# Performance work log

Hardware: AMD Instinct MI355X
Metric: run time of the kernel (lower is better)

Reference implementation:

```python
import jax, jax.numpy as jnp
import numpy as np

N_REP = 8      # N: repeated gelu(LN(linear)) blocks
M_LAYERS = 4   # M: transformer encoder layers
SEQ = 100
D = 4
FF = 2048      # PyTorch TransformerEncoderLayer default dim_feedforward
H = 4          # nhead; head_dim = 1


def _ln(x, g, b, axes):
    m = jnp.mean(x, axis=axes, keepdims=True)
    v = jnp.var(x, axis=axes, keepdims=True)
    return (x - m) / jnp.sqrt(v + 1e-5) * g + b


def _encoder_layer(x, Win, bi, Wout, bout, W1, b1, W2, b2, g1, be1, g2, be2):
    # x: [S, Nb, D] with S = batch_size (batch_first=False!), Nb = 100
    S, Nb, E = x.shape
    qkv = x @ Win.T + bi                      # [S, Nb, 3D]
    q, k, v = jnp.split(qkv, 3, axis=-1)
    qh = q.reshape(S, Nb, H, E // H)          # head_dim = 1, scale 1/sqrt(1)=1
    kh = k.reshape(S, Nb, H, E // H)
    vh = v.reshape(S, Nb, H, E // H)
    scores = jnp.einsum('snhd,tnhd->nhst', qh, kh)   # [Nb, H, S, S]
    attn = jax.nn.softmax(scores, axis=-1)
    o = jnp.einsum('nhst,tnhd->snhd', attn, vh).reshape(S, Nb, E)
    o = o @ Wout.T + bout
    x = _ln(x + o, g1, be1, (-1,))            # post-norm (norm_first=False)
    f = jax.nn.relu(x @ W1.T + b1) @ W2.T + b2
    return _ln(x + f, g2, be2, (-1,))


def setup_inputs() -> dict:
    key = jax.random.key(0)
    ks = jax.random.split(key, 24)
    B = 256
    d = {}
    d['x'] = jax.random.normal(ks[0], (B, SEQ, D), dtype=jnp.float32)
    # conv1: kernel_size=1, 1->1 channel -> scalar affine
    d['conv_w'] = jax.random.normal(ks[1], (), dtype=jnp.float32) * 0.5 + 1.0
    d['conv_b'] = jax.random.normal(ks[2], (), dtype=jnp.float32) * 0.1
    # shared 4x4 linear (self.liner) and LayerNorm([100,4])
    d['Wl'] = jax.random.normal(ks[3], (D, D), dtype=jnp.float32) * 0.5
    d['bl'] = jax.random.normal(ks[4], (D,), dtype=jnp.float32) * 0.1
    d['ln_g'] = jnp.ones((SEQ, D), dtype=jnp.float32)
    d['ln_b'] = jnp.zeros((SEQ, D), dtype=jnp.float32)
    # transformer encoder params, stacked over M layers
    s = 0.3
    d['Win'] = jax.random.normal(ks[5], (M_LAYERS, 3 * D, D), dtype=jnp.float32) * s
    d['bi'] = jax.random.normal(ks[6], (M_LAYERS, 3 * D), dtype=jnp.float32) * 0.05
    d['Wout'] = jax.random.normal(ks[7], (M_LAYERS, D, D), dtype=jnp.float32) * s
    d['bout'] = jax.random.normal(ks[8], (M_LAYERS, D), dtype=jnp.float32) * 0.05
    d['W1'] = jax.random.normal(ks[9], (M_LAYERS, FF, D), dtype=jnp.float32) * 0.05
    d['b1'] = jax.random.normal(ks[10], (M_LAYERS, FF), dtype=jnp.float32) * 0.05
    d['W2'] = jax.random.normal(ks[11], (M_LAYERS, D, FF), dtype=jnp.float32) * 0.02
    d['b2'] = jax.random.normal(ks[12], (M_LAYERS, D), dtype=jnp.float32) * 0.05
    d['g1'] = jnp.ones((M_LAYERS, D), dtype=jnp.float32)
    d['be1'] = jnp.zeros((M_LAYERS, D), dtype=jnp.float32)
    d['g2'] = jnp.ones((M_LAYERS, D), dtype=jnp.float32)
    d['be2'] = jnp.zeros((M_LAYERS, D), dtype=jnp.float32)
    return d


def reference(x, conv_w, conv_b, Wl, bl, ln_g, ln_b,
              Win, bi, Wout, bout, W1, b1, W2, b2, g1, be1, g2, be2):
    # per-channel kernel_size=1 conv == elementwise affine (same scalar for all 4 channels)
    h = x * conv_w + conv_b                   # [B, 100, 4]
    for _ in range(N_REP):
        h = jax.nn.gelu(_ln(h @ Wl.T + bl, ln_g, ln_b, (-2, -1)), approximate=False)
    h = h @ Wl.T + bl
    for i in range(M_LAYERS):
        h = _encoder_layer(h, Win[i], bi[i], Wout[i], bout[i], W1[i], b1[i],
                           W2[i], b2[i], g1[i], be1[i], g2[i], be2[i])
    h = h @ Wl.T + bl
    return jax.nn.softmax(h, axis=2)
```

## Files before the change

### kernel.cpp

```cpp
#include <hip/hip_runtime.h>
#include <math.h>

#define SEQ 100
#define BATCH 256
#define NREP 8
#define FFDIM 2048

__device__ __forceinline__ float wave_sum64(float v) {
    #pragma unroll
    for (int o = 32; o > 0; o >>= 1) v += __shfl_xor(v, o, 64);
    return v;
}

__global__ __launch_bounds__(128) void k_stageA(
    const float* __restrict__ x, const float* __restrict__ convw,
    const float* __restrict__ convb, const float* __restrict__ Wl,
    const float* __restrict__ bl, const float* __restrict__ lng,
    const float* __restrict__ lnb, float* __restrict__ X)
{
    const int b = blockIdx.x;
    const int r = threadIdx.x;
    const bool act = (r < SEQ);
    __shared__ float red[2][2];

    const float cw = convw[0], cb = convb[0];
    float W[4][4], B[4];
    #pragma unroll
    for (int j = 0; j < 4; ++j) {
        B[j] = bl[j];
        #pragma unroll
        for (int d = 0; d < 4; ++d) W[j][d] = Wl[j * 4 + d];
    }

    float h[4] = {0.f, 0.f, 0.f, 0.f};
    float g4[4] = {0.f, 0.f, 0.f, 0.f}, b4[4] = {0.f, 0.f, 0.f, 0.f};
    if (act) {
        float4 xr = *(const float4*)(x + (b * SEQ + r) * 4);
        h[0] = fmaf(xr.x, cw, cb); h[1] = fmaf(xr.y, cw, cb);
        h[2] = fmaf(xr.z, cw, cb); h[3] = fmaf(xr.w, cw, cb);
        float4 g = *(const float4*)(lng + r * 4);
        float4 bb = *(const float4*)(lnb + r * 4);
        g4[0] = g.x; g4[1] = g.y; g4[2] = g.z; g4[3] = g.w;
        b4[0] = bb.x; b4[1] = bb.y; b4[2] = bb.z; b4[3] = bb.w;
    }

    for (int it = 0; it < NREP; ++it) {
        float y[4] = {0.f, 0.f, 0.f, 0.f};
        float s1 = 0.f, s2 = 0.f;
        if (act) {
            #pragma unroll
            for (int j = 0; j < 4; ++j) {
                float yy = B[j];
                #pragma unroll
                for (int d = 0; d < 4; ++d) yy = fmaf(h[d], W[j][d], yy);
                y[j] = yy; s1 += yy; s2 = fmaf(yy, yy, s2);
            }
        }
        s1 = wave_sum64(s1);
        s2 = wave_sum64(s2);
        const int wid = threadIdx.x >> 6;
        if ((threadIdx.x & 63) == 0) { red[wid][0] = s1; red[wid][1] = s2; }
        __syncthreads();
        const float tS = red[0][0] + red[1][0];
        const float tQ = red[0][1] + red[1][1];
        __syncthreads();
        const float mean = tS * (1.0f / 400.0f);
        const float var  = tQ * (1.0f / 400.0f) - mean * mean;
        const float rstd = rsqrtf(var + 1e-5f);
        if (act) {
            #pragma unroll
            for (int j = 0; j < 4; ++j) {
                float v = fmaf((y[j] - mean) * rstd, g4[j], b4[j]);
                h[j] = 0.5f * v * (1.0f + erff(v * 0.70710678118654752f));
            }
        }
    }
    if (act) {
        float y[4];
        #pragma unroll
        for (int j = 0; j < 4; ++j) {
            float yy = B[j];
            #pragma unroll
            for (int d = 0; d < 4; ++d) yy = fmaf(h[d], W[j][d], yy);
            y[j] = yy;
        }
        *(float4*)(X + (b * SEQ + r) * 4) = make_float4(y[0], y[1], y[2], y[3]);
    }
}

__global__ __launch_bounds__(256) void k_attn(
    const float* __restrict__ X, float* __restrict__ O,
    const float* __restrict__ Win, const float* __restrict__ bi)
{
    const int n  = blockIdx.x;
    const int hd = blockIdx.y;
    const int s  = threadIdx.x;
    __shared__ float2 kv[256];
    __shared__ float red[4][2];

    float4 xr = *(const float4*)(X + (s * SEQ + n) * 4);
    const float* wq = Win + hd * 4;
    const float* wk = Win + (4 + hd) * 4;
    const float* wv = Win + (8 + hd) * 4;
    float q = bi[hd]     + xr.x*wq[0] + xr.y*wq[1] + xr.z*wq[2] + xr.w*wq[3];
    float k = bi[4 + hd] + xr.x*wk[0] + xr.y*wk[1] + xr.z*wk[2] + xr.w*wk[3];
    float v = bi[8 + hd] + xr.x*wv[0] + xr.y*wv[1] + xr.z*wv[2] + xr.w*wv[3];
    kv[s] = make_float2(k, v);

    float kmx = k, kmn = k;
    #pragma unroll
    for (int o = 32; o > 0; o >>= 1) {
        kmx = fmaxf(kmx, __shfl_xor(kmx, o, 64));
        kmn = fminf(kmn, __shfl_xor(kmn, o, 64));
    }
    const int wid = s >> 6;
    if ((s & 63) == 0) { red[wid][0] = kmx; red[wid][1] = kmn; }
    __syncthreads();
    kmx = fmaxf(fmaxf(red[0][0], red[1][0]), fmaxf(red[2][0], red[3][0]));
    kmn = fminf(fminf(red[0][1], red[1][1]), fminf(red[2][1], red[3][1]));

    const float m = (q >= 0.f) ? q * kmx : q * kmn;
    float den = 0.f, num = 0.f;
    #pragma unroll 8
    for (int t = 0; t < 256; ++t) {
        float2 kvt = kv[t];
        float p = __expf(fmaf(q, kvt.x, -m));
        den += p;
        num = fmaf(p, kvt.y, num);
    }
    O[(s * SEQ + n) * 4 + hd] = num / den;
}

__global__ __launch_bounds__(1024) void k_ffn(
    float* __restrict__ X, const float* __restrict__ O,
    const float* __restrict__ Wout, const float* __restrict__ bout,
    const float* __restrict__ W1, const float* __restrict__ b1,
    const float* __restrict__ W2, const float* __restrict__ b2,
    const float* __restrict__ g1, const float* __restrict__ be1,
    const float* __restrict__ g2, const float* __restrict__ be2)
{
    __shared__ float x1s[64][4];
    __shared__ float pacc[16][64][4];
    const int wid  = threadIdx.x >> 6;
    const int lane = threadIdx.x & 63;

    if (wid == 0) {
        const int g = blockIdx.x * 64 + lane;
        float4 xr = *(const float4*)(X + g * 4);
        float4 orow = *(const float4*)(O + g * 4);
        float xv[4] = {xr.x, xr.y, xr.z, xr.w};
        float ov[4] = {orow.x, orow.y, orow.z, orow.w};
        float rr[4];
        #pragma unroll
        for (int d = 0; d < 4; ++d) {
            float op = bout[d];
            #pragma unroll
            for (int e = 0; e < 4; ++e) op = fmaf(ov[e], Wout[d * 4 + e], op);
            rr[d] = xv[d] + op;
        }
        float mean = 0.25f * (rr[0] + rr[1] + rr[2] + rr[3]);
        float var = 0.f;
        #pragma unroll
        for (int d = 0; d < 4; ++d) { float dv = rr[d] - mean; var = fmaf(dv, dv, var); }
        float rstd = rsqrtf(0.25f * var + 1e-5f);
        #pragma unroll
        for (int d = 0; d < 4; ++d)
            x1s[lane][d] = fmaf((rr[d] - mean) * rstd, g1[d], be1[d]);
    }
    __syncthreads();

    const float x0 = x1s[lane][0], x1_ = x1s[lane][1];
    const float x2_ = x1s[lane][2], x3_ = x1s[lane][3];
    float a0 = 0.f, a1 = 0.f, a2 = 0.f, a3 = 0.f;
    const int fbase = __builtin_amdgcn_readfirstlane(wid) * 128;
    #pragma unroll 4
    for (int j = 0; j < 128; ++j) {
        const int f = fbase + j;
        const float w0 = W1[f * 4 + 0], w1 = W1[f * 4 + 1];
        const float w2 = W1[f * 4 + 2], w3 = W1[f * 4 + 3];
        float hh = b1[f];
        hh = fmaf(x0, w0, hh); hh = fmaf(x1_, w1, hh);
        hh = fmaf(x2_, w2, hh); hh = fmaf(x3_, w3, hh);
        hh = fmaxf(hh, 0.f);
        a0 = fmaf(hh, W2[0 * FFDIM + f], a0);
        a1 = fmaf(hh, W2[1 * FFDIM + f], a1);
        a2 = fmaf(hh, W2[2 * FFDIM + f], a2);
        a3 = fmaf(hh, W2[3 * FFDIM + f], a3);
    }
    pacc[wid][lane][0] = a0; pacc[wid][lane][1] = a1;
    pacc[wid][lane][2] = a2; pacc[wid][lane][3] = a3;
    __syncthreads();

    if (threadIdx.x < 256) {
        const int r = threadIdx.x >> 2, d = threadIdx.x & 3;
        float s = b2[d];
        #pragma unroll
        for (int w = 0; w < 16; ++w) s += pacc[w][r][d];
        float val = x1s[r][d] + s;
        float sum = val + __shfl_xor(val, 1, 64);
        sum += __shfl_xor(sum, 2, 64);
        const float mean = 0.25f * sum;
        const float dv = val - mean;
        float qq = dv * dv;
        float qs = qq + __shfl_xor(qq, 1, 64);
        qs += __shfl_xor(qs, 2, 64);
        const float rstd = rsqrtf(0.25f * qs + 1e-5f);
        X[(blockIdx.x * 64 + r) * 4 + d] = fmaf(dv * rstd, g2[d], be2[d]);
    }
}

__global__ __launch_bounds__(256) void k_final(
    const float* __restrict__ X, const float* __restrict__ Wl,
    const float* __restrict__ bl, float* __restrict__ out)
{
    const int g = blockIdx.x * 256 + threadIdx.x;
    float4 xr = *(const float4*)(X + g * 4);
    float xv[4] = {xr.x, xr.y, xr.z, xr.w};
    float y[4];
    #pragma unroll
    for (int j = 0; j < 4; ++j) {
        float yy = bl[j];
        #pragma unroll
        for (int d = 0; d < 4; ++d) yy = fmaf(xv[d], Wl[j * 4 + d], yy);
        y[j] = yy;
    }
    float m = fmaxf(fmaxf(y[0], y[1]), fmaxf(y[2], y[3]));
    float e[4], s = 0.f;
    #pragma unroll
    for (int j = 0; j < 4; ++j) { e[j] = __expf(y[j] - m); s += e[j]; }
    const float inv = 1.0f / s;
    *(float4*)(out + g * 4) =
        make_float4(e[0] * inv, e[1] * inv, e[2] * inv, e[3] * inv);
}

extern "C" void kernel_launch(void* const* d_in, const int* in_sizes, int n_in,
                              void* d_out, int out_size, void* d_ws, size_t ws_size,
                              hipStream_t stream)
{
    const float* x     = (const float*)d_in[0];
    const float* convw = (const float*)d_in[1];
    const float* convb = (const float*)d_in[2];
    const float* Wl    = (const float*)d_in[3];
    const float* bl    = (const float*)d_in[4];
    const float* lng   = (const float*)d_in[5];
    const float* lnb   = (const float*)d_in[6];
    const float* Win   = (const float*)d_in[7];
    const float* bi    = (const float*)d_in[8];
    const float* Wout  = (const float*)d_in[9];
    const float* bout  = (const float*)d_in[10];
    const float* W1    = (const float*)d_in[11];
    const float* b1    = (const float*)d_in[12];
    const float* W2    = (const float*)d_in[13];
    const float* b2    = (const float*)d_in[14];
    const float* g1    = (const float*)d_in[15];
    const float* be1   = (const float*)d_in[16];
    const float* g2    = (const float*)d_in[17];
    const float* be2   = (const float*)d_in[18];

    float* X = (float*)d_ws;
    float* O = X + BATCH * SEQ * 4;
    float* out = (float*)d_out;

    k_stageA<<<BATCH, 128, 0, stream>>>(x, convw, convb, Wl, bl, lng, lnb, X);
    for (int l = 0; l < 4; ++l) {
        k_attn<<<dim3(SEQ, 4), 256, 0, stream>>>(X, O, Win + l * 48, bi + l * 12);
        k_ffn<<<400, 1024, 0, stream>>>(X, O,
            Wout + l * 16, bout + l * 4,
            W1 + l * FFDIM * 4, b1 + l * FFDIM,
            W2 + l * 4 * FFDIM, b2 + l * 4,
            g1 + l * 4, be1 + l * 4, g2 + l * 4, be2 + l * 4);
    }
    k_final<<<SEQ, 256, 0, stream>>>(X, Wl, bl, out);
}
```

Before: 128.0 us.

## Fuse all stages into one persistent kernel with software grid barriers

Replaces the ten separate kernel launches (stage A, four attention plus FFN pairs, final softmax) with a single persistent kernel of 256 blocks that separates phases with an atomic-counter grid barrier. Stage A now uses a single wave with two rows per lane, so no block-level reduction is needed. Attention slots and FFN rows are remapped so each block handles up to two attention slots and 100 rows, with two rows per lane in the FFN. This removes launch gaps and the per-launch tail, at the cost of spin-wait barriers, the assumption that all 256 blocks are co-resident, and fewer blocks in the FFN phase (256 instead of 400).

```diff
diff --git a/kernel.cpp b/kernel.cpp
--- a/kernel.cpp
+++ b/kernel.cpp
@@ -1,274 +1,312 @@
 #include <hip/hip_runtime.h>
 #include <math.h>
 
-#define SEQ 100
-#define BATCH 256
-#define NREP 8
-#define FFDIM 2048
-
-__device__ __forceinline__ float wave_sum64(float v) {
-    #pragma unroll
-    for (int o = 32; o > 0; o >>= 1) v += __shfl_xor(v, o, 64);
-    return v;
+#define SEQ   100
+#define NREP  8
+#define FFD   2048
+#define NBLK  256
+#define RSQRT2 0.70710678118654752440f
+
+__device__ __forceinline__ float wsum(float v) {
+#pragma unroll
+  for (int o = 32; o > 0; o >>= 1) v += __shfl_xor(v, o, 64);
+  return v;
 }
 
-__global__ __launch_bounds__(128) void k_stageA(
-    const float* __restrict__ x, const float* __restrict__ convw,
-    const float* __restrict__ convb, const float* __restrict__ Wl,
-    const float* __restrict__ bl, const float* __restrict__ lng,
-    const float* __restrict__ lnb, float* __restrict__ X)
+__device__ __forceinline__ void gbar(unsigned* cnt, unsigned* gen) {
+  __syncthreads();
+  if (threadIdx.x == 0) {
+    __threadfence();
+    unsigned g0 = __hip_atomic_load(gen, __ATOMIC_RELAXED, __HIP_MEMORY_SCOPE_AGENT);
+    unsigned a  = __hip_atomic_fetch_add(cnt, 1u, __ATOMIC_ACQ_REL, __HIP_MEMORY_SCOPE_AGENT);
+    if (a == (unsigned)(NBLK - 1)) {
+      __hip_atomic_store(cnt, 0u, __ATOMIC_RELAXED, __HIP_MEMORY_SCOPE_AGENT);
+      __hip_atomic_fetch_add(gen, 1u, __ATOMIC_RELEASE, __HIP_MEMORY_SCOPE_AGENT);
+    } else {
+      while (__hip_atomic_load(gen, __ATOMIC_ACQUIRE, __HIP_MEMORY_SCOPE_AGENT) == g0)
+        __builtin_amdgcn_s_sleep(2);
+    }
+    __threadfence();
+  }
+  __syncthreads();
+}
+
+__global__ __launch_bounds__(1024) void k_fused(
+    const float* __restrict__ x,
+    const float* __restrict__ convw, const float* __restrict__ convb,
+    const float* __restrict__ Wl,  const float* __restrict__ bl,
+    const float* __restrict__ lng, const float* __restrict__ lnb,
+    const float* __restrict__ Win, const float* __restrict__ bi,
+    const float* __restrict__ Wout,const float* __restrict__ bout,
+    const float* __restrict__ W1,  const float* __restrict__ b1,
+    const float* __restrict__ W2,  const float* __restrict__ b2,
+    const float* __restrict__ g1,  const float* __restrict__ be1,
+    const float* __restrict__ g2,  const float* __restrict__ be2,
+    float* __restrict__ X, float* __restrict__ O,
+    unsigned* __restrict__ barc, unsigned* __restrict__ barg,
+    float* __restrict__ out)
 {
-    const int b = blockIdx.x;
-    const int r = threadIdx.x;
-    const bool act = (r < SEQ);
-    __shared__ float red[2][2];
-
+  __shared__ float2 kvs[4][256];
+  __shared__ float  kred[4][4][2];
+  __shared__ float  x1s[100][4];
+  __shared__ float  pacc[16][100][4];
+
+  const int t    = threadIdx.x;
+  const int b    = blockIdx.x;
+  const int lane = t & 63;
+  const int wv   = t >> 6;
+
+  if (t < 64) {
     const float cw = convw[0], cb = convb[0];
     float W[4][4], B[4];
-    #pragma unroll
+#pragma unroll
     for (int j = 0; j < 4; ++j) {
-        B[j] = bl[j];
-        #pragma unroll
-        for (int d = 0; d < 4; ++d) W[j][d] = Wl[j * 4 + d];
-    }
-
-    float h[4] = {0.f, 0.f, 0.f, 0.f};
-    float g4[4] = {0.f, 0.f, 0.f, 0.f}, b4[4] = {0.f, 0.f, 0.f, 0.f};
+      B[j] = bl[j];
+#pragma unroll
+      for (int d = 0; d < 4; ++d) W[j][d] = Wl[j * 4 + d];
+    }
+    const bool act = lane < 50;
+    float h[2][4] = {{0.f,0.f,0.f,0.f},{0.f,0.f,0.f,0.f}};
+    float gg[2][4] = {{0.f}}, eb[2][4] = {{0.f}};
     if (act) {
+#pragma unroll
+      for (int p = 0; p < 2; ++p) {
+        const int r = lane * 2 + p;
         float4 xr = *(const float4*)(x + (b * SEQ + r) * 4);
-        h[0] = fmaf(xr.x, cw, cb); h[1] = fmaf(xr.y, cw, cb);
-        h[2] = fmaf(xr.z, cw, cb); h[3] = fmaf(xr.w, cw, cb);
-        float4 g = *(const float4*)(lng + r * 4);
-        float4 bb = *(const float4*)(lnb + r * 4);
-        g4[0] = g.x; g4[1] = g.y; g4[2] = g.z; g4[3] = g.w;
-        b4[0] = bb.x; b4[1] = bb.y; b4[2] = bb.z; b4[3] = bb.w;
-    }
-
+        h[p][0] = fmaf(xr.x, cw, cb); h[p][1] = fmaf(xr.y, cw, cb);
+        h[p][2] = fmaf(xr.z, cw, cb); h[p][3] = fmaf(xr.w, cw, cb);
+        float4 gv = *(const float4*)(lng + r * 4);
+        float4 bv = *(const float4*)(lnb + r * 4);
+        gg[p][0] = gv.x; gg[p][1] = gv.y; gg[p][2] = gv.z; gg[p][3] = gv.w;
+        eb[p][0] = bv.x; eb[p][1] = bv.y; eb[p][2] = bv.z; eb[p][3] = bv.w;
+      }
+    }
     for (int it = 0; it < NREP; ++it) {
-        float y[4] = {0.f, 0.f, 0.f, 0.f};
-        float s1 = 0.f, s2 = 0.f;
-        if (act) {
-            #pragma unroll
-            for (int j = 0; j < 4; ++j) {
-                float yy = B[j];
-                #pragma unroll
-                for (int d = 0; d < 4; ++d) yy = fmaf(h[d], W[j][d], yy);
-                y[j] = yy; s1 += yy; s2 = fmaf(yy, yy, s2);
-            }
+      float y[2][4] = {{0.f,0.f,0.f,0.f},{0.f,0.f,0.f,0.f}};
+      float s1 = 0.f, s2 = 0.f;
+      if (act) {
+#pragma unroll
+        for (int p = 0; p < 2; ++p)
+#pragma unroll
+          for (int j = 0; j < 4; ++j) {
+            float yy = B[j];
+#pragma unroll
+            for (int d = 0; d < 4; ++d) yy = fmaf(h[p][d], W[j][d], yy);
+            y[p][j] = yy; s1 += yy; s2 = fmaf(yy, yy, s2);
+          }
+      }
+      s1 = wsum(s1); s2 = wsum(s2);
+      const float mean = s1 * (1.0f / 400.0f);
+      const float var  = s2 * (1.0f / 400.0f) - mean * mean;
+      const float rstd = rsqrtf(var + 1e-5f);
+      if (act) {
+#pragma unroll
+        for (int p = 0; p < 2; ++p)
+#pragma unroll
+          for (int j = 0; j < 4; ++j) {
+            float vv = fmaf((y[p][j] - mean) * rstd, gg[p][j], eb[p][j]);
+            h[p][j] = 0.5f * vv * (1.0f + erff(vv * RSQRT2));
+          }
+      }
+    }
+    if (act) {
+#pragma unroll
+      for (int p = 0; p < 2; ++p) {
+        float yy[4];
+#pragma unroll
+        for (int j = 0; j < 4; ++j) {
+          float a = B[j];
+#pragma unroll
+          for (int d = 0; d < 4; ++d) a = fmaf(h[p][d], W[j][d], a);
+          yy[j] = a;
         }
-        s1 = wave_sum64(s1);
-        s2 = wave_sum64(s2);
-        const int wid = threadIdx.x >> 6;
-        if ((threadIdx.x & 63) == 0) { red[wid][0] = s1; red[wid][1] = s2; }
-        __syncthreads();
-        const float tS = red[0][0] + red[1][0];
-        const float tQ = red[0][1] + red[1][1];
-        __syncthreads();
-        const float mean = tS * (1.0f / 400.0f);
-        const float var  = tQ * (1.0f / 400.0f) - mean * mean;
-        const float rstd = rsqrtf(var + 1e-5f);
-        if (act) {
-            #pragma unroll
-            for (int j = 0; j < 4; ++j) {
-                float v = fmaf((y[j] - mean) * rstd, g4[j], b4[j]);
-                h[j] = 0.5f * v * (1.0f + erff(v * 0.70710678118654752f));
-            }
-        }
-    }
-    if (act) {
-        float y[4];
-        #pragma unroll
-        for (int j = 0; j < 4; ++j) {
-            float yy = B[j];
-            #pragma unroll
-            for (int d = 0; d < 4; ++d) yy = fmaf(h[d], W[j][d], yy);
-            y[j] = yy;
-        }
-        *(float4*)(X + (b * SEQ + r) * 4) = make_float4(y[0], y[1], y[2], y[3]);
-    }
-}
-
-__global__ __launch_bounds__(256) void k_attn(
-    const float* __restrict__ X, float* __restrict__ O,
-    const float* __restrict__ Win, const float* __restrict__ bi)
-{
-    const int n  = blockIdx.x;
-    const int hd = blockIdx.y;
-    const int s  = threadIdx.x;
-    __shared__ float2 kv[256];
-    __shared__ float red[4][2];
-
-    float4 xr = *(const float4*)(X + (s * SEQ + n) * 4);
-    const float* wq = Win + hd * 4;
-    const float* wk = Win + (4 + hd) * 4;
-    const float* wv = Win + (8 + hd) * 4;
-    float q = bi[hd]     + xr.x*wq[0] + xr.y*wq[1] + xr.z*wq[2] + xr.w*wq[3];
-    float k = bi[4 + hd] + xr.x*wk[0] + xr.y*wk[1] + xr.z*wk[2] + xr.w*wk[3];
-    float v = bi[8 + hd] + xr.x*wv[0] + xr.y*wv[1] + xr.z*wv[2] + xr.w*wv[3];
-    kv[s] = make_float2(k, v);
-
-    float kmx = k, kmn = k;
-    #pragma unroll
-    for (int o = 32; o > 0; o >>= 1) {
+        *(float4*)(X + (b * SEQ + lane * 2 + p) * 4) =
+            make_float4(yy[0], yy[1], yy[2], yy[3]);
+      }
+    }
+  }
+  gbar(barc, barg);
+
+  for (int l = 0; l < 4; ++l) {
+    {
+      const float* Wa = Win + l * 48;
+      const float* ba = bi + l * 12;
+      const int g    = t >> 8;
+      const int s    = t & 255;
+      const int slot = b + 256 * g;
+      const int sc   = slot < 400 ? slot : 399;
+      const int n    = sc % 100;
+      const int hd   = sc / 100;
+      float4 xr = *(const float4*)(X + (s * SEQ + n) * 4);
+      const float* wq = Wa + hd * 4;
+      const float* wk = Wa + (4 + hd) * 4;
+      const float* wvp = Wa + (8 + hd) * 4;
+      float q = ba[hd]   + xr.x*wq[0] + xr.y*wq[1] + xr.z*wq[2] + xr.w*wq[3];
+      float k = ba[4+hd] + xr.x*wk[0] + xr.y*wk[1] + xr.z*wk[2] + xr.w*wk[3];
+      float v = ba[8+hd] + xr.x*wvp[0]+ xr.y*wvp[1]+ xr.z*wvp[2]+ xr.w*wvp[3];
+      kvs[g][s] = make_float2(k, v);
+      float kmx = k, kmn = k;
+#pragma unroll
+      for (int o = 32; o > 0; o >>= 1) {
         kmx = fmaxf(kmx, __shfl_xor(kmx, o, 64));
         kmn = fminf(kmn, __shfl_xor(kmn, o, 64));
-    }
-    const int wid = s >> 6;
-    if ((s & 63) == 0) { red[wid][0] = kmx; red[wid][1] = kmn; }
-    __syncthreads();
-    kmx = fmaxf(fmaxf(red[0][0], red[1][0]), fmaxf(red[2][0], red[3][0]));
-    kmn = fminf(fminf(red[0][1], red[1][1]), fminf(red[2][1], red[3][1]));
-
-    const float m = (q >= 0.f) ? q * kmx : q * kmn;
-    float den = 0.f, num = 0.f;
-    #pragma unroll 8
-    for (int t = 0; t < 256; ++t) {
-        float2 kvt = kv[t];
-        float p = __expf(fmaf(q, kvt.x, -m));
-        den += p;
-        num = fmaf(p, kvt.y, num);
-    }
-    O[(s * SEQ + n) * 4 + hd] = num / den;
-}
-
-__global__ __launch_bounds__(1024) void k_ffn(
-    float* __restrict__ X, const float* __restrict__ O,
-    const float* __restrict__ Wout, const float* __restrict__ bout,
-    const float* __restrict__ W1, const float* __restrict__ b1,
-    const float* __restrict__ W2, const float* __restrict__ b2,
-    const float* __restrict__ g1, const float* __restrict__ be1,
-    const float* __restrict__ g2, const float* __restrict__ be2)
-{
-    __shared__ float x1s[64][4];
-    __shared__ float pacc[16][64][4];
-    const int wid  = threadIdx.x >> 6;
-    const int lane = threadIdx.x & 63;
-
-    if (wid == 0) {
-        const int g = blockIdx.x * 64 + lane;
-        float4 xr = *(const float4*)(X + g * 4);
-        float4 orow = *(const float4*)(O + g * 4);
+      }
+      if ((t & 63) == 0) { kred[g][(t >> 6) & 3][0] = kmx; kred[g][(t >> 6) & 3][1] = kmn; }
+      __syncthreads();
+      if (slot < 400) {
+        kmx = fmaxf(fmaxf(kred[g][0][0], kred[g][1][0]),
+                    fmaxf(kred[g][2][0], kred[g][3][0]));
+        kmn = fminf(fminf(kred[g][0][1], kred[g][1][1]),
+                    fminf(kred[g][2][1], kred[g][3][1]));
+        const float m = (q >= 0.f) ? q * kmx : q * kmn;
+        float den = 0.f, num = 0.f;
+#pragma unroll 8
+        for (int t2 = 0; t2 < 256; ++t2) {
+          float2 kt = kvs[g][t2];
+          float p = __expf(fmaf(q, kt.x, -m));
+          den += p;
+          num = fmaf(p, kt.y, num);
+        }
+        O[(s * SEQ + n) * 4 + hd] = num / den;
+      }
+    }
+    gbar(barc, barg);
+
+    {
+      const float* W1l = W1 + l * FFD * 4;
+      const float* b1l = b1 + l * FFD;
+      const float* W2l = W2 + l * 4 * FFD;
+      const float* b2l = b2 + l * 4;
+      const float* Wo  = Wout + l * 16;
+      const float* bo  = bout + l * 4;
+      const float* g1l = g1 + l * 4;  const float* e1l = be1 + l * 4;
+      const float* g2l = g2 + l * 4;  const float* e2l = be2 + l * 4;
+
+      if (t < 100) {
+        const int gr = b * SEQ + t;
+        float4 xr = *(const float4*)(X + gr * 4);
+        float4 od = *(const float4*)(O + gr * 4);
         float xv[4] = {xr.x, xr.y, xr.z, xr.w};
-        float ov[4] = {orow.x, orow.y, orow.z, orow.w};
+        float ov[4] = {od.x, od.y, od.z, od.w};
         float rr[4];
-        #pragma unroll
+#pragma unroll
         for (int d = 0; d < 4; ++d) {
-            float op = bout[d];
-            #pragma unroll
-            for (int e = 0; e < 4; ++e) op = fmaf(ov[e], Wout[d * 4 + e], op);
-            rr[d] = xv[d] + op;
+          float op = bo[d];
+#pragma unroll
+          for (int e = 0; e < 4; ++e) op = fmaf(ov[e], Wo[d * 4 + e], op);
+          rr[d] = xv[d] + op;
         }
         float mean = 0.25f * (rr[0] + rr[1] + rr[2] + rr[3]);
         float var = 0.f;
-        #pragma unroll
+#pragma unroll
         for (int d = 0; d < 4; ++d) { float dv = rr[d] - mean; var = fmaf(dv, dv, var); }
         float rstd = rsqrtf(0.25f * var + 1e-5f);
-        #pragma unroll
+#pragma unroll
         for (int d = 0; d < 4; ++d)
-            x1s[lane][d] = fmaf((rr[d] - mean) * rstd, g1[d], be1[d]);
-    }
-    __syncthreads();
-
-    const float x0 = x1s[lane][0], x1_ = x1s[lane][1];
-    const float x2_ = x1s[lane][2], x3_ = x1s[lane][3];
-    float a0 = 0.f, a1 = 0.f, a2 = 0.f, a3 = 0.f;
-    const int fbase = __builtin_amdgcn_readfirstlane(wid) * 128;
-    #pragma unroll 4
-    for (int j = 0; j < 128; ++j) {
-        const int f = fbase + j;
-        const float w0 = W1[f * 4 + 0], w1 = W1[f * 4 + 1];
-        const float w2 = W1[f * 4 + 2], w3 = W1[f * 4 + 3];
-        float hh = b1[f];
-        hh = fmaf(x0, w0, hh); hh = fmaf(x1_, w1, hh);
-        hh = fmaf(x2_, w2, hh); hh = fmaf(x3_, w3, hh);
-        hh = fmaxf(hh, 0.f);
-        a0 = fmaf(hh, W2[0 * FFDIM + f], a0);
-        a1 = fmaf(hh, W2[1 * FFDIM + f], a1);
-        a2 = fmaf(hh, W2[2 * FFDIM + f], a2);
-        a3 = fmaf(hh, W2[3 * FFDIM + f], a3);
-    }
-    pacc[wid][lane][0] = a0; pacc[wid][lane][1] = a1;
-    pacc[wid][lane][2] = a2; pacc[wid][lane][3] = a3;
-    __syncthreads();
-
-    if (threadIdx.x < 256) {
-        const int r = threadIdx.x >> 2, d = threadIdx.x & 3;
-        float s = b2[d];
-        #pragma unroll
-        for (int w = 0; w < 16; ++w) s += pacc[w][r][d];
-        float val = x1s[r][d] + s;
-        float sum = val + __shfl_xor(val, 1, 64);
-        sum += __shfl_xor(sum, 2, 64);
+          x1s[t][d] = fmaf((rr[d] - mean) * rstd, g1l[d], e1l[d]);
+      }
+      __syncthreads();
+
+      const int fb = __builtin_amdgcn_readfirstlane(wv) * 128;
+      const int rB = 64 + (lane < 36 ? lane : 35);
+      const float xA0 = x1s[lane][0], xA1 = x1s[lane][1];
+      const float xA2 = x1s[lane][2], xA3 = x1s[lane][3];
+      const float xB0 = x1s[rB][0], xB1 = x1s[rB][1];
+      const float xB2 = x1s[rB][2], xB3 = x1s[rB][3];
+      float aA0=0.f,aA1=0.f,aA2=0.f,aA3=0.f;
+      float aB0=0.f,aB1=0.f,aB2=0.f,aB3=0.f;
+#pragma unroll 4
+      for (int j = 0; j < 128; ++j) {
+        const int f = fb + j;
+        const float4 w1v = *(const float4*)(W1l + f * 4);
+        const float bb  = b1l[f];
+        const float w20 = W2l[f],           w21 = W2l[FFD + f];
+        const float w22 = W2l[2 * FFD + f], w23 = W2l[3 * FFD + f];
+        float hA = fmaf(xA3, w1v.w, fmaf(xA2, w1v.z, fmaf(xA1, w1v.y, fmaf(xA0, w1v.x, bb))));
+        hA = fmaxf(hA, 0.f);
+        aA0 = fmaf(hA, w20, aA0); aA1 = fmaf(hA, w21, aA1);
+        aA2 = fmaf(hA, w22, aA2); aA3 = fmaf(hA, w23, aA3);
+        float hB = fmaf(xB3, w1v.w, fmaf(xB2, w1v.z, fmaf(xB1, w1v.y, fmaf(xB0, w1v.x, bb))));
+        hB = fmaxf(hB, 0.f);
+        aB0 = fmaf(hB, w20, aB0); aB1 = fmaf(hB, w21, aB1);
+        aB2 = fmaf(hB, w22, aB2); aB3 = fmaf(hB, w23, aB3);
+      }
+      *(float4*)&pacc[wv][lane][0] = make_float4(aA0, aA1, aA2, aA3);
+      if (lane < 36)
+        *(float4*)&pacc[wv][64 + lane][0] = make_float4(aB0, aB1, aB2, aB3);
+      __syncthreads();
+
+      if (t < 400) {
+        const int r = t >> 2, d = t & 3;
+        float sacc = b2l[d];
+#pragma unroll
+        for (int w = 0; w < 16; ++w) sacc += pacc[w][r][d];
+        float val = x1s[r][d] + sacc;
+        float sum = val + __shfl_xor(val, 1, 64); sum += __shfl_xor(sum, 2, 64);
         const float mean = 0.25f * sum;
         const float dv = val - mean;
         float qq = dv * dv;
-        float qs = qq + __shfl_xor(qq, 1, 64);
-        qs += __shfl_xor(qs, 2, 64);
+        float qs = qq + __shfl_xor(qq, 1, 64); qs += __shfl_xor(qs, 2, 64);
         const float rstd = rsqrtf(0.25f * qs + 1e-5f);
-        X[(blockIdx.x * 64 + r) * 4 + d] = fmaf(dv * rstd, g2[d], be2[d]);
-    }
-}
-
-__global__ __launch_bounds__(256) void k_final(
-    const float* __restrict__ X, const float* __restrict__ Wl,
-    const float* __restrict__ bl, float* __restrict__ out)
-{
-    const int g = blockIdx.x * 256 + threadIdx.x;
-    float4 xr = *(const float4*)(X + g * 4);
+        X[(b * SEQ + r) * 4 + d] = fmaf(dv * rstd, g2l[d], e2l[d]);
+      }
+    }
+    if (l < 3) gbar(barc, barg);
+    else __syncthreads();
+  }
+
+  if (t < 100) {
+    const int gr = b * SEQ + t;
+    float4 xr = *(const float4*)(X + gr * 4);
     float xv[4] = {xr.x, xr.y, xr.z, xr.w};
     float y[4];
-    #pragma unroll
+#pragma unroll
     for (int j = 0; j < 4; ++j) {
-        float yy = bl[j];
-        #pragma unroll
-        for (int d = 0; d < 4; ++d) yy = fmaf(xv[d], Wl[j * 4 + d], yy);
-        y[j] = yy;
+      float yy = bl[j];
+#pragma unroll
+      for (int d = 0; d < 4; ++d) yy = fmaf(xv[d], Wl[j * 4 + d], yy);
+      y[j] = yy;
     }
     float m = fmaxf(fmaxf(y[0], y[1]), fmaxf(y[2], y[3]));
     float e[4], s = 0.f;
-    #pragma unroll
+#pragma unroll
     for (int j = 0; j < 4; ++j) { e[j] = __expf(y[j] - m); s += e[j]; }
     const float inv = 1.0f / s;
-    *(float4*)(out + g * 4) =
-        make_float4(e[0] * inv, e[1] * inv, e[2] * inv, e[3] * inv);
+    *(float4*)(out + gr * 4) = make_float4(e[0]*inv, e[1]*inv, e[2]*inv, e[3]*inv);
+  }
 }
 
 extern "C" void kernel_launch(void* const* d_in, const int* in_sizes, int n_in,
                               void* d_out, int out_size, void* d_ws, size_t ws_size,
                               hipStream_t stream)
 {
-    const float* x     = (const float*)d_in[0];
-    const float* convw = (const float*)d_in[1];
-    const float* convb = (const float*)d_in[2];
-    const float* Wl    = (const float*)d_in[3];
-    const float* bl    = (const float*)d_in[4];
-    const float* lng   = (const float*)d_in[5];
-    const float* lnb   = (const float*)d_in[6];
-    const float* Win   = (const float*)d_in[7];
-    const float* bi    = (const float*)d_in[8];
-    const float* Wout  = (const float*)d_in[9];
-    const float* bout  = (const float*)d_in[10];
-    const float* W1    = (const float*)d_in[11];
-    const float* b1    = (const float*)d_in[12];
-    const float* W2    = (const float*)d_in[13];
-    const float* b2    = (const float*)d_in[14];
-    const float* g1    = (const float*)d_in[15];
-    const float* be1   = (const float*)d_in[16];
-    const float* g2    = (const float*)d_in[17];
-    const float* be2   = (const float*)d_in[18];
-
-    float* X = (float*)d_ws;
-    float* O = X + BATCH * SEQ * 4;
-    float* out = (float*)d_out;
-
-    k_stageA<<<BATCH, 128, 0, stream>>>(x, convw, convb, Wl, bl, lng, lnb, X);
-    for (int l = 0; l < 4; ++l) {
-        k_attn<<<dim3(SEQ, 4), 256, 0, stream>>>(X, O, Win + l * 48, bi + l * 12);
-        k_ffn<<<400, 1024, 0, stream>>>(X, O,
-            Wout + l * 16, bout + l * 4,
-            W1 + l * FFDIM * 4, b1 + l * FFDIM,
-            W2 + l * 4 * FFDIM, b2 + l * 4,
-            g1 + l * 4, be1 + l * 4, g2 + l * 4, be2 + l * 4);
-    }
-    k_final<<<SEQ, 256, 0, stream>>>(X, Wl, bl, out);
+  const float* x     = (const float*)d_in[0];
+  const float* convw = (const float*)d_in[1];
+  const float* convb = (const float*)d_in[2];
+  const float* Wl    = (const float*)d_in[3];
+  const float* bl    = (const float*)d_in[4];
+  const float* lng   = (const float*)d_in[5];
+  const float* lnb   = (const float*)d_in[6];
+  const float* Win   = (const float*)d_in[7];
+  const float* bi    = (const float*)d_in[8];
+  const float* Wout  = (const float*)d_in[9];
+  const float* bout  = (const float*)d_in[10];
+  const float* W1    = (const float*)d_in[11];
+  const float* b1    = (const float*)d_in[12];
+  const float* W2    = (const float*)d_in[13];
+  const float* b2    = (const float*)d_in[14];
+  const float* g1    = (const float*)d_in[15];
+  const float* be1   = (const float*)d_in[16];
+  const float* g2    = (const float*)d_in[17];
+  const float* be2   = (const float*)d_in[18];
+
+  float* X = (float*)d_ws;
+  float* O = X + 256 * SEQ * 4;
+  unsigned* bar = (unsigned*)((char*)d_ws + (1 << 20));
+  hipMemsetAsync(bar, 0, 8, stream);
+
+  k_fused<<<NBLK, 1024, 0, stream>>>(x, convw, convb, Wl, bl, lng, lnb,
+                                     Win, bi, Wout, bout, W1, b1, W2, b2,
+                                     g1, be1, g2, be2, X, O, bar, bar + 1,
+                                     (float*)d_out);
 }
```

New measurement: 430.2 us. 236% more time.
